# Kernel optimization log

Hardware: AMD Instinct MI355X
Metric: run time of the kernel (lower is better)

## Reference

```python
import jax, jax.numpy as jnp
import numpy as np

DIM = 1024
HEADS = 16
HEAD_DIM = DIM // HEADS
MLP = 4 * DIM
EPS = 1e-5


def layer_norm(x, g, b):
    mu = jnp.mean(x, axis=-1, keepdims=True)
    var = jnp.var(x, axis=-1, keepdims=True)
    return (x - mu) * jax.lax.rsqrt(var + EPS) * g + b


def rope_cos_sin(n, d):
    inv_freq = 1.0 / (10000.0 ** (jnp.arange(0, d, 2, dtype=jnp.float32) / d))
    t = jnp.arange(n, dtype=jnp.float32)
    freqs = jnp.outer(t, inv_freq)          # [N, d/2]
    emb = jnp.concatenate([freqs, freqs], -1)  # [N, d]
    return jnp.cos(emb), jnp.sin(emb)


def rotate_half(x):
    x1, x2 = x[..., ::2], x[..., 1::2]
    return jnp.concatenate([-x2, x1], axis=-1)


def setup_inputs() -> dict:
    key = jax.random.key(0)
    ks = jax.random.split(key, 16)
    B, N = 2, 2048
    s = lambda fan_in: 1.0 / np.sqrt(fan_in)
    inp = {
        "x": jax.random.normal(ks[0], (B, N, DIM), jnp.float32),
        "t_emb": jax.random.normal(ks[1], (B, DIM), jnp.float32),
        "norm1_g": jnp.ones((DIM,), jnp.float32),
        "norm1_b": jnp.zeros((DIM,), jnp.float32),
        "Wq": jax.random.normal(ks[2], (DIM, DIM), jnp.float32) * s(DIM),
        "Wk": jax.random.normal(ks[3], (DIM, DIM), jnp.float32) * s(DIM),
        "Wv": jax.random.normal(ks[4], (DIM, DIM), jnp.float32) * s(DIM),
        "Wo": jax.random.normal(ks[5], (DIM, DIM), jnp.float32) * s(DIM),
        "norm2_g": jnp.ones((DIM,), jnp.float32),
        "norm2_b": jnp.zeros((DIM,), jnp.float32),
        "W1": jax.random.normal(ks[6], (DIM, MLP), jnp.float32) * s(DIM),
        "W2": jax.random.normal(ks[7], (MLP, DIM), jnp.float32) * s(MLP),
        "ada_W": jax.random.normal(ks[8], (DIM, 6 * DIM), jnp.float32) * s(DIM),
        "ada_b": jnp.zeros((6 * DIM,), jnp.float32),
    }
    return inp


def reference(x, t_emb, norm1_g, norm1_b, Wq, Wk, Wv, Wo,
              norm2_g, norm2_b, W1, W2, ada_W, ada_b):
    B, N, C = x.shape
    H, D = HEADS, HEAD_DIM
    scale = D ** -0.5

    mod = jax.nn.silu(t_emb) @ ada_W + ada_b          # [B, 6C]
    (shift_msa, scale_msa, gate_msa,
     shift_mlp, scale_mlp, gate_mlp) = jnp.split(mod, 6, axis=-1)

    xn = layer_norm(x, norm1_g, norm1_b) * (1 + scale_msa[:, None, :]) + shift_msa[:, None, :]

    q = (xn @ Wq).reshape(B, N, H, D).transpose(0, 2, 1, 3)  # [B,H,N,D]
    k = (xn @ Wk).reshape(B, N, H, D).transpose(0, 2, 1, 3)
    v = (xn @ Wv).reshape(B, N, H, D).transpose(0, 2, 1, 3)

    cos, sin = rope_cos_sin(N, D)                     # [N, D]
    q = q * cos + rotate_half(q) * sin
    k = k * cos + rotate_half(k) * sin

    attn = jnp.einsum('bhnd,bhmd->bhnm', q, k) * scale  # explicit O(N^2) scores
    attn = jax.nn.softmax(attn, axis=-1)
    out = jnp.einsum('bhnm,bhmd->bhnd', attn, v)

    out = out.transpose(0, 2, 1, 3).reshape(B, N, C) @ Wo
    x = x + gate_msa[:, None, :] * out

    xn = layer_norm(x, norm2_g, norm2_b) * (1 + scale_mlp[:, None, :]) + shift_mlp[:, None, :]
    mlp = jax.nn.gelu(xn @ W1, approximate=False) @ W2
    x = x + gate_mlp[:, None, :] * mlp
    return x
```

## Files before the change

kernel.cpp:

```cpp
#include <hip/hip_runtime.h>
#include <math.h>

#define BB    2
#define NN    2048
#define CDIM  1024
#define HEADS 16
#define HDIM  64
#define MLPD  4096
#define MODC  6144
#define EPSV  1e-5f
#define LOG2E 1.4426950408889634f
#define MSPLIT 16

typedef __attribute__((ext_vector_type(8))) short s8v;
typedef __attribute__((ext_vector_type(4))) float f4v;

__device__ inline unsigned short f2bf(float f) {
  union { float f; unsigned u; } v; v.f = f;
  unsigned r = v.u + 0x7FFFu + ((v.u >> 16) & 1u);
  return (unsigned short)(r >> 16);
}
__device__ inline float bf2f(unsigned short h) {
  union { unsigned u; float f; } v; v.u = ((unsigned)h) << 16;
  return v.f;
}

__global__ __launch_bounds__(256) void mod_part(
    const float* __restrict__ t_emb, const float* __restrict__ ada_W,
    float* __restrict__ part) {
  int j = blockIdx.x * 256 + threadIdx.x;
  int b = blockIdx.y, ks = blockIdx.z;
  __shared__ float st[64];
  if (threadIdx.x < 64) {
    float v = t_emb[b * CDIM + ks * 64 + threadIdx.x];
    st[threadIdx.x] = v / (1.0f + expf(-v));
  }
  __syncthreads();
  float acc = 0.f;
  const float* wp = ada_W + (size_t)(ks * 64) * MODC + j;
  #pragma unroll 8
  for (int i = 0; i < 64; ++i) acc += st[i] * wp[(size_t)i * MODC];
  part[((size_t)ks * BB + b) * MODC + j] = acc;
}

__global__ __launch_bounds__(256) void mod_reduce(
    const float* __restrict__ part, const float* __restrict__ ada_b,
    float* __restrict__ mod) {
  int idx = blockIdx.x * 256 + threadIdx.x;
  int b = idx / MODC, j = idx % MODC;
  float a = ada_b[j];
  #pragma unroll
  for (int s = 0; s < MSPLIT; ++s) a += part[((size_t)s * BB + b) * MODC + j];
  mod[(size_t)b * MODC + j] = a;
}

__device__ inline float wave_sum64(float v) {
  for (int o = 32; o > 0; o >>= 1) v += __shfl_down(v, o, 64);
  return v;
}

__global__ __launch_bounds__(256) void ln_mod_bf16(
    const float* __restrict__ x, const float* __restrict__ g,
    const float* __restrict__ bta, const float* __restrict__ mod,
    int shift_off, int scale_off, unsigned short* __restrict__ out) {
  int r = blockIdx.x;
  int b = r / NN;
  int t = threadIdx.x;
  const float* xr = x + (size_t)r * CDIM;
  float4 xv = ((const float4*)xr)[t];
  float s  = xv.x + xv.y + xv.z + xv.w;
  float s2 = xv.x*xv.x + xv.y*xv.y + xv.z*xv.z + xv.w*xv.w;
  __shared__ float ws1[4], ws2[4];
  float sw = wave_sum64(s), s2w = wave_sum64(s2);
  int lane = t & 63, wid = t >> 6;
  if (lane == 0) { ws1[wid] = sw; ws2[wid] = s2w; }
  __syncthreads();
  float mu  = (ws1[0] + ws1[1] + ws1[2] + ws1[3]) * (1.0f / CDIM);
  float var = (ws2[0] + ws2[1] + ws2[2] + ws2[3]) * (1.0f / CDIM) - mu * mu;
  float rstd = rsqrtf(var + EPSV);
  const float* mods = mod + (size_t)b * MODC;
  float4 gv = ((const float4*)g)[t];
  float4 bv = ((const float4*)bta)[t];
  float4 sc = ((const float4*)(mods + scale_off))[t];
  float4 sh = ((const float4*)(mods + shift_off))[t];
  ushort4 ov;
  ov.x = f2bf(((xv.x - mu) * rstd * gv.x + bv.x) * (1.0f + sc.x) + sh.x);
  ov.y = f2bf(((xv.y - mu) * rstd * gv.y + bv.y) * (1.0f + sc.y) + sh.y);
  ov.z = f2bf(((xv.z - mu) * rstd * gv.z + bv.z) * (1.0f + sc.z) + sh.z);
  ov.w = f2bf(((xv.w - mu) * rstd * gv.w + bv.w) * (1.0f + sc.w) + sh.w);
  ((ushort4*)(out + (size_t)r * CDIM))[t] = ov;
}

__global__ __launch_bounds__(256) void wcast_all(
    const float* __restrict__ Wq, const float* __restrict__ Wk,
    const float* __restrict__ Wv, const float* __restrict__ Wo,
    const float* __restrict__ W1, const float* __restrict__ W2,
    unsigned short* __restrict__ Wqkvt, unsigned short* __restrict__ Wot,
    unsigned short* __restrict__ W1t, unsigned short* __restrict__ W2t) {
  int bid = blockIdx.x;
  const float* W; unsigned short* Wt; int K, N, t;
  if (bid < 4096) {
    int m = bid >> 10;
    t = bid & 1023;
    K = CDIM; N = CDIM;
    W  = (m == 0) ? Wq : (m == 1) ? Wk : (m == 2) ? Wv : Wo;
    Wt = (m == 3) ? Wot : (Wqkvt + (size_t)m * CDIM * CDIM);
  } else if (bid < 8192) {
    t = bid - 4096; K = CDIM; N = MLPD; W = W1; Wt = W1t;
  } else {
    t = bid - 8192; K = MLPD; N = CDIM; W = W2; Wt = W2t;
  }
  int ntiles = N >> 5;
  int n0 = (t % ntiles) * 32, k0 = (t / ntiles) * 32;
  __shared__ float tile[32][33];
  int tx = threadIdx.x & 31, ty = threadIdx.x >> 5;
  #pragma unroll
  for (int p = 0; p < 4; ++p)
    tile[ty + p * 8][tx] = W[(size_t)(k0 + ty + p * 8) * N + n0 + tx];
  __syncthreads();
  #pragma unroll
  for (int p = 0; p < 4; ++p)
    Wt[(size_t)(n0 + ty + p * 8) * K + k0 + tx] = f2bf(tile[tx][ty + p * 8]);
}

__global__ __launch_bounds__(1024) void mfma_gemm_big(
    const unsigned short* __restrict__ A,
    const unsigned short* __restrict__ Bt,
    int M, int N, int K,
    unsigned short* __restrict__ Ob, unsigned short* __restrict__ Ob2,
    unsigned short* __restrict__ Ob3, int mode) {
  __shared__ unsigned short SH[3 * 16384];
  int tid = threadIdx.x;
  int wave = tid >> 6, lane = tid & 63;
  int quad = lane >> 4, l15 = lane & 15;
  int m0 = blockIdx.y * 128, n0 = blockIdx.x * 128;
  int pos = wave & 7;
  int om = pos >> 1, on = pos & 1;
  int ks = wave >> 3;

  f4v acc[2][4] = {};

  int srow = lane >> 3;
  int ksrc = ((lane & 7) ^ (lane >> 3)) << 3;
  const int nt = K >> 6;

  #define STAGE_BIG(T, BUF)                                                    \
    {                                                                          \
      int k0_ = (T) << 6;                                                      \
      unsigned short* dsta = SH + (BUF) * 16384 + wave * 512;                  \
      const unsigned short* ga =                                               \
          A + (size_t)(m0 + 8 * wave + srow) * K + k0_ + ksrc;                 \
      __builtin_amdgcn_global_load_lds(                                        \
          (const __attribute__((address_space(1))) unsigned int*)(const void*)ga, \
          (__attribute__((address_space(3))) unsigned int*)(void*)dsta,        \
          16, 0, 0);                                                           \
      const unsigned short* gb =                                               \
          Bt + (size_t)(n0 + 8 * wave + srow) * K + k0_ + ksrc;                \
      __builtin_amdgcn_global_load_lds(                                        \
          (const __attribute__((address_space(1))) unsigned int*)(const void*)gb, \
          (__attribute__((address_space(3))) unsigned int*)(void*)(dsta + 8192), \
          16, 0, 0);                                                           \
    }

  STAGE_BIG(0, 0);
  STAGE_BIG(1, 1);
  asm volatile("s_waitcnt vmcnt(2)" ::: "memory");
  __syncthreads();

  int kx = (ks * 32 + quad * 8) ^ ((l15 & 7) << 3);

  int rbuf = 0, sbuf = 2;
  for (int t = 0; t < nt; ++t) {
    if (t + 2 < nt) STAGE_BIG(t + 2, sbuf);

    const unsigned short* base = SH + rbuf * 16384;
    s8v af[2], bf[4];
    #pragma unroll
    for (int i = 0; i < 2; ++i)
      af[i] = *(const s8v*)(base + (om * 32 + i * 16 + l15) * 64 + kx);
    #pragma unroll
    for (int j = 0; j < 4; ++j)
      bf[j] = *(const s8v*)(base + 8192 + (on * 64 + j * 16 + l15) * 64 + kx);
    #pragma unroll
    for (int i = 0; i < 2; ++i)
      #pragma unroll
      for (int j = 0; j < 4; ++j)
        acc[i][j] = __builtin_amdgcn_mfma_f32_16x16x32_bf16(
            af[i], bf[j], acc[i][j], 0, 0, 0);

    if (t + 2 < nt) {
      asm volatile("s_waitcnt vmcnt(2)" ::: "memory");
    } else if (t + 1 < nt) {
      asm volatile("s_waitcnt vmcnt(0)" ::: "memory");
    }
    __syncthreads();
    rbuf = (rbuf == 2) ? 0 : rbuf + 1;
    sbuf = (sbuf == 2) ? 0 : sbuf + 1;
  }
  #undef STAGE_BIG

  float* red = (float*)SH;
  if (wave >= 8) {
    int rb = (wave - 8) * 2304 + lane * 36;
    #pragma unroll
    for (int i = 0; i < 2; ++i)
      #pragma unroll
      for (int j = 0; j < 4; ++j)
        *(f4v*)(red + rb + (i * 4 + j) * 4) = acc[i][j];
  }
  __syncthreads();
  if (wave < 8) {
    int rb = wave * 2304 + lane * 36;
    #pragma unroll
    for (int i = 0; i < 2; ++i)
      #pragma unroll
      for (int j = 0; j < 4; ++j)
        acc[i][j] += *(const f4v*)(red + rb + (i * 4 + j) * 4);
    #pragma unroll
    for (int i = 0; i < 2; ++i) {
      int rbase = m0 + om * 32 + i * 16 + quad * 4;
      #pragma unroll
      for (int j = 0; j < 4; ++j) {
        int c = n0 + on * 64 + j * 16 + l15;
        #pragma unroll
        for (int rg = 0; rg < 4; ++rg) {
          int r = rbase + rg;
          float v = acc[i][j][rg];
          if (mode == 0) {
            unsigned short* dst = (c < 1024) ? Ob : ((c < 2048) ? Ob2 : Ob3);
            dst[(size_t)r * 1024 + (c & 1023)] = f2bf(v);
          } else {
            v = 0.5f * v * (1.0f + erff(v * 0.70710678118f));
            Ob[(size_t)r * N + c] = f2bf(v);
          }
        }
      }
    }
  }
}

__global__ __launch_bounds__(1024) void mfma_gemm_res(
    const unsigned short* __restrict__ A,
    const unsigned short* __restrict__ Bt,
    int M, int N, int K,
    float* __restrict__ O0,
    const float* __restrict__ res, const float* __restrict__ mod,
    int gate_off) {
  __shared__ unsigned short SH[3 * 16384];
  int tid = threadIdx.x;
  int wave = tid >> 6, lane = tid & 63;
  int quad = lane >> 4, l15 = lane & 15;
  int m0 = blockIdx.y * 128, n0 = blockIdx.x * 128;
  int pos = wave & 7;
  int om = pos >> 1, on = pos & 1;
  int ks = wave >> 3;

  f4v acc[2][4] = {};

  int srow = lane >> 3;
  int ksrc = ((lane & 7) ^ (lane >> 3)) << 3;
  const int nt = K >> 6;

  #define STAGE_RES(T, BUF)                                                    \
    {                                                                          \
      int k0_ = (T) << 6;                                                      \
      unsigned short* dsta = SH + (BUF) * 16384 + wave * 512;                  \
      const unsigned short* ga =                                               \
          A + (size_t)(m0 + 8 * wave + srow) * K + k0_ + ksrc;                 \
      __builtin_amdgcn_global_load_lds(                                        \
          (const __attribute__((address_space(1))) unsigned int*)(const void*)ga, \
          (__attribute__((address_space(3))) unsigned int*)(void*)dsta,        \
          16, 0, 0);                                                           \
      const unsigned short* gb =                                               \
          Bt + (size_t)(n0 + 8 * wave + srow) * K + k0_ + ksrc;                \
      __builtin_amdgcn_global_load_lds(                                        \
          (const __attribute__((address_space(1))) unsigned int*)(const void*)gb, \
          (__attribute__((address_space(3))) unsigned int*)(void*)(dsta + 8192), \
          16, 0, 0);                                                           \
    }

  STAGE_RES(0, 0);
  STAGE_RES(1, 1);
  asm volatile("s_waitcnt vmcnt(2)" ::: "memory");
  __syncthreads();

  int kx = (ks * 32 + quad * 8) ^ ((l15 & 7) << 3);

  int rbuf = 0, sbuf = 2;
  for (int t = 0; t < nt; ++t) {
    if (t + 2 < nt) STAGE_RES(t + 2, sbuf);

    const unsigned short* base = SH + rbuf * 16384;
    s8v af[2], bf[4];
    #pragma unroll
    for (int i = 0; i < 2; ++i)
      af[i] = *(const s8v*)(base + (om * 32 + i * 16 + l15) * 64 + kx);
    #pragma unroll
    for (int j = 0; j < 4; ++j)
      bf[j] = *(const s8v*)(base + 8192 + (on * 64 + j * 16 + l15) * 64 + kx);
    #pragma unroll
    for (int i = 0; i < 2; ++i)
      #pragma unroll
      for (int j = 0; j < 4; ++j)
        acc[i][j] = __builtin_amdgcn_mfma_f32_16x16x32_bf16(
            af[i], bf[j], acc[i][j], 0, 0, 0);

    if (t + 2 < nt) {
      asm volatile("s_waitcnt vmcnt(2)" ::: "memory");
    } else if (t + 1 < nt) {
      asm volatile("s_waitcnt vmcnt(0)" ::: "memory");
    }
    __syncthreads();
    rbuf = (rbuf == 2) ? 0 : rbuf + 1;
    sbuf = (sbuf == 2) ? 0 : sbuf + 1;
  }
  #undef STAGE_RES

  float* red = (float*)SH;
  if (wave >= 8) {
    int rb = (wave - 8) * 2304 + lane * 36;
    #pragma unroll
    for (int i = 0; i < 2; ++i)
      #pragma unroll
      for (int j = 0; j < 4; ++j)
        *(f4v*)(red + rb + (i * 4 + j) * 4) = acc[i][j];
  }
  __syncthreads();
  if (wave < 8) {
    int rb = wave * 2304 + lane * 36;
    #pragma unroll
    for (int i = 0; i < 2; ++i)
      #pragma unroll
      for (int j = 0; j < 4; ++j)
        acc[i][j] += *(const f4v*)(red + rb + (i * 4 + j) * 4);
    #pragma unroll
    for (int i = 0; i < 2; ++i) {
      int rbase = m0 + om * 32 + i * 16 + quad * 4;
      #pragma unroll
      for (int j = 0; j < 4; ++j) {
        int c = n0 + on * 64 + j * 16 + l15;
        #pragma unroll
        for (int rg = 0; rg < 4; ++rg) {
          int r = rbase + rg;
          int bb2 = r >> 11;
          O0[(size_t)r * N + c] =
              res[(size_t)r * N + c] + mod[bb2 * MODC + gate_off + c] * acc[i][j][rg];
        }
      }
    }
  }
}

__global__ __launch_bounds__(256) void rope_qk(
    unsigned short* __restrict__ qb, const unsigned short* __restrict__ kb,
    unsigned short* __restrict__ kpack, float qscale) {
  int r = blockIdx.x;
  int b = r / NN, n = r % NN;
  int t = threadIdx.x;
  int isK = blockIdx.y;
  const unsigned short* src = isK ? kb : qb;
  float scale = isK ? 1.0f : qscale;
  __shared__ float row[CDIM];
  __shared__ float csv[32], snv[32];
  if (t < 32) {
    float invf = powf(10000.0f, -(float)t / 32.0f);
    float sn, cs;
    sincosf((float)n * invf, &sn, &cs);
    csv[t] = cs * scale; snv[t] = sn * scale;
  }
  const unsigned short* qr = src + (size_t)r * CDIM;
  ushort4 xv = ((const ushort4*)qr)[t];
  row[t * 4 + 0] = bf2f(xv.x);
  row[t * 4 + 1] = bf2f(xv.y);
  row[t * 4 + 2] = bf2f(xv.z);
  row[t * 4 + 3] = bf2f(xv.w);
  __syncthreads();
  unsigned short o[4];
  int c0 = t * 4;
  #pragma unroll
  for (int q4 = 0; q4 < 4; ++q4) {
    int c = c0 + q4;
    int h = c >> 6, d = c & 63;
    int i = d & 31;
    float rh = (d < 32) ? -row[h * 64 + 2 * d + 1] : row[h * 64 + 2 * (d - 32)];
    o[q4] = f2bf(row[c] * csv[i] + rh * snv[i]);
  }
  if (!isK) {
    ((ushort4*)(qb + (size_t)r * CDIM))[t] = make_ushort4(o[0], o[1], o[2], o[3]);
  } else {
    int h = c0 >> 6, d0 = c0 & 63;
    int half = d0 >> 5, quad = (d0 >> 3) & 3, j0 = d0 & 7;
    int bh = b * HEADS + h;
    int tt = n >> 6, kt = (n >> 4) & 3, l15 = n & 15;
    int lane = quad * 16 + l15;
    size_t off = ((((size_t)bh * 32 + tt) * 8 + kt * 2 + half) * 64 + lane) * 8 + j0;
    unsigned int lo = (unsigned)o[0] | ((unsigned)o[1] << 16);
    unsigned int hi = (unsigned)o[2] | ((unsigned)o[3] << 16);
    *(uint2*)(kpack + off) = make_uint2(lo, hi);
  }
}

__global__ __launch_bounds__(256) void vtrans_pack(
    const unsigned short* __restrict__ vrow, unsigned short* __restrict__ vpack) {
  int t = blockIdx.x;
  int bh = blockIdx.y;
  int b = bh >> 4, h = bh & 15;
  __shared__ unsigned short L[64 * 72];
  int tid = threadIdx.x;
  #pragma unroll
  for (int p = 0; p < 2; ++p) {
    int c = tid + p * 256;
    int key = c >> 3, dc = (c & 7) * 8;
    *(s8v*)(L + key * 72 + dc) =
        *(const s8v*)(vrow + (size_t)(b * NN + t * 64 + key) * CDIM + h * HDIM + dc);
  }
  __syncthreads();
  #pragma unroll
  for (int p = 0; p < 2; ++p) {
    int o = tid + p * 256;
    int f = o >> 6, lane = o & 63;
    int dt = f >> 1, half = f & 1, quad = lane >> 4, l15 = lane & 15;
    int d = dt * 16 + l15;
    unsigned short tmp[8];
    #pragma unroll
    for (int j = 0; j < 8; ++j) {
      int key = (j & 3) * 16 + half * 8 + quad * 2 + (j >> 2);
      tmp[j] = L[key * 72 + d];
    }
    *(s8v*)(vpack + ((((size_t)bh * 32 + t) * 8 + f) * 64 + lane) * 8) = *(s8v*)tmp;
  }
}

__global__ __launch_bounds__(512, 4) void fattn_pack(
    const unsigned short* __restrict__ qb,
    const unsigned short* __restrict__ kpack,
    const unsigned short* __restrict__ vpack,
    unsigned short* __restrict__ ob) {
  int bid = blockIdx.x;
  int qt = bid >> 5, bh = bid & 31;
  int b = bh >> 4, h = bh & 15;
  int tid = threadIdx.x;
  int wave = tid >> 6, lane = tid & 63;
  int quad = lane >> 4, l15 = lane & 15;

  __shared__ unsigned short smem[16384 + 8 * 1152];
  unsigned short* Pw = smem + 16384 + wave * 1152;

  int n0 = qt * 128;
  int qrow = n0 + wave * 16 + l15;
  s8v qf[2];
  {
    const unsigned short* qp = qb + (size_t)(b * NN + qrow) * CDIM + h * HDIM;
    qf[0] = *(const s8v*)(qp + quad * 8);
    qf[1] = *(const s8v*)(qp + 32 + quad * 8);
  }

  f4v acc[4] = {};
  float m_i[4], l_i[4];
  #pragma unroll
  for (int r = 0; r < 4; ++r) { m_i[r] = -1e30f; l_i[r] = 0.f; }

  const unsigned short* ksrc = kpack + (size_t)bh * 131072 + wave * 512 + lane * 8;
  const unsigned short* vsrc = vpack + (size_t)bh * 131072 + wave * 512 + lane * 8;

  #define STAGE_ATT(T, BUF)                                                    \
    {                                                                          \
      __builtin_amdgcn_global_load_lds(                                        \
          (const __attribute__((address_space(1))) unsigned int*)(const void*)(ksrc + (size_t)(T) * 4096), \
          (__attribute__((address_space(3))) unsigned int*)(void*)(smem + (BUF) * 8192 + wave * 512), \
          16, 0, 0);                                                           \
      __builtin_amdgcn_global_load_lds(                                        \
          (const __attribute__((address_space(1))) unsigned int*)(const void*)(vsrc + (size_t)(T) * 4096), \
          (__attribute__((address_space(3))) unsigned int*)(void*)(smem + (BUF) * 8192 + 4096 + wave * 512), \
          16, 0, 0);                                                           \
    }

  STAGE_ATT(0, 0);
  asm volatile("s_waitcnt vmcnt(0)" ::: "memory");
  __syncthreads();

  int buf = 0;
  for (int t = 0; t < NN / 64; ++t) {
    if (t + 1 < NN / 64) STAGE_ATT(t + 1, buf ^ 1);

    const unsigned short* kb_ = smem + buf * 8192 + lane * 8;
    const unsigned short* vb_ = kb_ + 4096;
    s8v kf[8], vf[8];
    #pragma unroll
    for (int f = 0; f < 8; ++f) kf[f] = *(const s8v*)(kb_ + f * 512);
    #pragma unroll
    for (int f = 0; f < 8; ++f) vf[f] = *(const s8v*)(vb_ + f * 512);

    f4v s4[4] = {};
    #pragma unroll
    for (int kt = 0; kt < 4; ++kt) {
      s4[kt] = __builtin_amdgcn_mfma_f32_16x16x32_bf16(qf[0], kf[kt * 2], s4[kt], 0, 0, 0);
      s4[kt] = __builtin_amdgcn_mfma_f32_16x16x32_bf16(qf[1], kf[kt * 2 + 1], s4[kt], 0, 0, 0);
    }

    #pragma unroll
    for (int r = 0; r < 4; ++r) {
      float mv = fmaxf(fmaxf(s4[0][r], s4[1][r]), fmaxf(s4[2][r], s4[3][r]));
      #pragma unroll
      for (int msk = 1; msk < 16; msk <<= 1)
        mv = fmaxf(mv, __shfl_xor(mv, msk, 64));
      float mnew = fmaxf(m_i[r], mv);
      float alpha = __builtin_amdgcn_exp2f(m_i[r] - mnew);
      m_i[r] = mnew;
      float ls = 0.f;
      #pragma unroll
      for (int kt = 0; kt < 4; ++kt) {
        float p = __builtin_amdgcn_exp2f(s4[kt][r] - mnew);
        s4[kt][r] = p;
        ls += p;
      }
      l_i[r] = l_i[r] * alpha + ls;
      acc[0][r] *= alpha; acc[1][r] *= alpha;
      acc[2][r] *= alpha; acc[3][r] *= alpha;
    }

    #pragma unroll
    for (int r = 0; r < 4; ++r) {
      unsigned int lo = (__float_as_uint(s4[0][r]) >> 16) |
                        (__float_as_uint(s4[1][r]) & 0xffff0000u);
      unsigned int hi = (__float_as_uint(s4[2][r]) >> 16) |
                        (__float_as_uint(s4[3][r]) & 0xffff0000u);
      *(uint2*)(Pw + (quad * 4 + r) * 72 + l15 * 4) = make_uint2(lo, hi);
    }

    s8v pf0 = *(const s8v*)(Pw + l15 * 72 + quad * 8);
    s8v pf1 = *(const s8v*)(Pw + l15 * 72 + 32 + quad * 8);

    #pragma unroll
    for (int dt = 0; dt < 4; ++dt) {
      acc[dt] = __builtin_amdgcn_mfma_f32_16x16x32_bf16(pf0, vf[dt * 2], acc[dt], 0, 0, 0);
      acc[dt] = __builtin_amdgcn_mfma_f32_16x16x32_bf16(pf1, vf[dt * 2 + 1], acc[dt], 0, 0, 0);
    }

    if (t + 1 < NN / 64) {
      asm volatile("s_waitcnt vmcnt(0)" ::: "memory");
      __syncthreads();
      buf ^= 1;
    }
  }
  #undef STAGE_ATT

  #pragma unroll
  for (int r = 0; r < 4; ++r) {
    float l = l_i[r];
    #pragma unroll
    for (int msk = 1; msk < 16; msk <<= 1)
      l += __shfl_xor(l, msk, 64);
    float inv = 1.0f / l;
    size_t row = (size_t)(b * NN + n0 + wave * 16 + quad * 4 + r);
    unsigned short* op = ob + row * CDIM + h * HDIM;
    #pragma unroll
    for (int dt = 0; dt < 4; ++dt)
      op[dt * 16 + l15] = f2bf(acc[dt][r] * inv);
  }
}

extern "C" void kernel_launch(void* const* d_in, const int* in_sizes, int n_in,
                              void* d_out, int out_size, void* d_ws, size_t ws_size,
                              hipStream_t stream) {
  const float* x    = (const float*)d_in[0];
  const float* temb = (const float*)d_in[1];
  const float* n1g  = (const float*)d_in[2];
  const float* n1b  = (const float*)d_in[3];
  const float* Wq   = (const float*)d_in[4];
  const float* Wk   = (const float*)d_in[5];
  const float* Wv   = (const float*)d_in[6];
  const float* Wo   = (const float*)d_in[7];
  const float* n2g  = (const float*)d_in[8];
  const float* n2b  = (const float*)d_in[9];
  const float* W1   = (const float*)d_in[10];
  const float* W2   = (const float*)d_in[11];
  const float* adaW = (const float*)d_in[12];
  const float* adab = (const float*)d_in[13];
  float* out = (float*)d_out;

  const size_t TOK = (size_t)BB * NN * CDIM;
  float* wsf = (float*)d_ws;
  float* mod     = wsf;
  float* modpart = wsf + 16384;
  unsigned short* tokb  = (unsigned short*)(wsf + 16384 + MSPLIT * BB * MODC);
  unsigned short* qb    = tokb + TOK;
  unsigned short* kb    = qb + TOK;
  unsigned short* kpack = kb + TOK;
  unsigned short* vpack = kpack + TOK;
  unsigned short* Wqkvt = vpack + TOK;
  unsigned short* Wot   = Wqkvt + 3 * CDIM * CDIM;
  unsigned short* W1t   = Wot + CDIM * CDIM;
  unsigned short* W2t   = W1t + CDIM * MLPD;
  unsigned short* h1b   = W2t + MLPD * CDIM;
  unsigned short* vrow  = h1b;
  float* x1 = (float*)qb;

  const int M = BB * NN;

  mod_part<<<dim3(MODC / 256, BB, MSPLIT), 256, 0, stream>>>(temb, adaW, modpart);
  mod_reduce<<<dim3(BB * MODC / 256), 256, 0, stream>>>(modpart, adab, mod);
  ln_mod_bf16<<<dim3(M), 256, 0, stream>>>(x, n1g, n1b, mod, 0, 1024, tokb);

  wcast_all<<<dim3(12288), 256, 0, stream>>>(
      Wq, Wk, Wv, Wo, W1, W2, Wqkvt, Wot, W1t, W2t);

  mfma_gemm_big<<<dim3(24, 32), 1024, 0, stream>>>(
      tokb, Wqkvt, M, 3 * CDIM, CDIM, qb, kb, vrow, 0);

  rope_qk<<<dim3(M, 2), 256, 0, stream>>>(qb, kb, kpack, 0.125f * LOG2E);

  vtrans_pack<<<dim3(NN / 64, BB * HEADS), 256, 0, stream>>>(vrow, vpack);

  fattn_pack<<<dim3((NN / 128) * BB * HEADS), 512, 0, stream>>>(
      qb, kpack, vpack, tokb);

  mfma_gemm_res<<<dim3(CDIM / 128, M / 128), 1024, 0, stream>>>(
      tokb, Wot, M, CDIM, CDIM, x1, x, mod, 2048);

  ln_mod_bf16<<<dim3(M), 256, 0, stream>>>(x1, n2g, n2b, mod, 3072, 4096, tokb);

  mfma_gemm_big<<<dim3(MLPD / 128, M / 128), 1024, 0, stream>>>(
      tokb, W1t, M, MLPD, CDIM, h1b, nullptr, nullptr, 1);

  mfma_gemm_res<<<dim3(CDIM / 128, M / 128), 1024, 0, stream>>>(
      h1b, W2t, M, CDIM, MLPD, out, x1, mod, 5120);
}
```

Measured before the change: 428.7 us.

## Process two 16-row query fragments per wave in flash attention

Each wave now handles 32 query rows instead of 16, so a block covers 256 queries and reuses every staged K/V tile for twice as many rows. This halves the number of blocks and the total global-to-LDS K/V traffic. In exchange it raises register use per thread (launch bounds occupancy hint dropped) and per-block LDS for the P buffers. The grid shrinks to 256 blocks, which is close to the CU count and may leave less latency hiding.

Result: no change. 428.8 us (+0.0%).

```diff
diff --git a/kernel.cpp b/kernel.cpp
--- a/kernel.cpp
+++ b/kernel.cpp
@@ -431,7 +431,7 @@
   }
 }
 
-__global__ __launch_bounds__(512, 4) void fattn_pack(
+__global__ __launch_bounds__(512) void fattn_pack(
     const unsigned short* __restrict__ qb,
     const unsigned short* __restrict__ kpack,
     const unsigned short* __restrict__ vpack,
@@ -443,22 +443,25 @@
   int wave = tid >> 6, lane = tid & 63;
   int quad = lane >> 4, l15 = lane & 15;
 
-  __shared__ unsigned short smem[16384 + 8 * 1152];
-  unsigned short* Pw = smem + 16384 + wave * 1152;
-
-  int n0 = qt * 128;
-  int qrow = n0 + wave * 16 + l15;
-  s8v qf[2];
-  {
+  __shared__ unsigned short smem[16384 + 8 * 2304];
+  unsigned short* Pw = smem + 16384 + wave * 2304;
+
+  int n0 = qt * 256;
+  s8v qf[2][2];
+  #pragma unroll
+  for (int fq = 0; fq < 2; ++fq) {
+    int qrow = n0 + wave * 32 + fq * 16 + l15;
     const unsigned short* qp = qb + (size_t)(b * NN + qrow) * CDIM + h * HDIM;
-    qf[0] = *(const s8v*)(qp + quad * 8);
-    qf[1] = *(const s8v*)(qp + 32 + quad * 8);
-  }
-
-  f4v acc[4] = {};
-  float m_i[4], l_i[4];
-  #pragma unroll
-  for (int r = 0; r < 4; ++r) { m_i[r] = -1e30f; l_i[r] = 0.f; }
+    qf[fq][0] = *(const s8v*)(qp + quad * 8);
+    qf[fq][1] = *(const s8v*)(qp + 32 + quad * 8);
+  }
+
+  f4v acc[2][4] = {};
+  float m_i[2][4], l_i[2][4];
+  #pragma unroll
+  for (int fq = 0; fq < 2; ++fq)
+    #pragma unroll
+    for (int r = 0; r < 4; ++r) { m_i[fq][r] = -1e30f; l_i[fq][r] = 0.f; }
 
   const unsigned short* ksrc = kpack + (size_t)bh * 131072 + wave * 512 + lane * 8;
   const unsigned short* vsrc = vpack + (size_t)bh * 131072 + wave * 512 + lane * 8;
@@ -484,57 +487,72 @@
     if (t + 1 < NN / 64) STAGE_ATT(t + 1, buf ^ 1);
 
     const unsigned short* kb_ = smem + buf * 8192 + lane * 8;
-    const unsigned short* vb_ = kb_ + 4096;
-    s8v kf[8], vf[8];
-    #pragma unroll
-    for (int f = 0; f < 8; ++f) kf[f] = *(const s8v*)(kb_ + f * 512);
-    #pragma unroll
-    for (int f = 0; f < 8; ++f) vf[f] = *(const s8v*)(vb_ + f * 512);
-
-    f4v s4[4] = {};
-    #pragma unroll
-    for (int kt = 0; kt < 4; ++kt) {
-      s4[kt] = __builtin_amdgcn_mfma_f32_16x16x32_bf16(qf[0], kf[kt * 2], s4[kt], 0, 0, 0);
-      s4[kt] = __builtin_amdgcn_mfma_f32_16x16x32_bf16(qf[1], kf[kt * 2 + 1], s4[kt], 0, 0, 0);
-    }
-
-    #pragma unroll
-    for (int r = 0; r < 4; ++r) {
-      float mv = fmaxf(fmaxf(s4[0][r], s4[1][r]), fmaxf(s4[2][r], s4[3][r]));
-      #pragma unroll
-      for (int msk = 1; msk < 16; msk <<= 1)
-        mv = fmaxf(mv, __shfl_xor(mv, msk, 64));
-      float mnew = fmaxf(m_i[r], mv);
-      float alpha = __builtin_amdgcn_exp2f(m_i[r] - mnew);
-      m_i[r] = mnew;
-      float ls = 0.f;
-      #pragma unroll
-      for (int kt = 0; kt < 4; ++kt) {
-        float p = __builtin_amdgcn_exp2f(s4[kt][r] - mnew);
-        s4[kt][r] = p;
-        ls += p;
+    f4v s4[2][4];
+    {
+      s8v kf[8];
+      #pragma unroll
+      for (int f = 0; f < 8; ++f) kf[f] = *(const s8v*)(kb_ + f * 512);
+      #pragma unroll
+      for (int fq = 0; fq < 2; ++fq)
+        #pragma unroll
+        for (int kt = 0; kt < 4; ++kt) {
+          f4v z = {};
+          z = __builtin_amdgcn_mfma_f32_16x16x32_bf16(qf[fq][0], kf[kt * 2], z, 0, 0, 0);
+          z = __builtin_amdgcn_mfma_f32_16x16x32_bf16(qf[fq][1], kf[kt * 2 + 1], z, 0, 0, 0);
+          s4[fq][kt] = z;
+        }
+    }
+
+    #pragma unroll
+    for (int fq = 0; fq < 2; ++fq)
+      #pragma unroll
+      for (int r = 0; r < 4; ++r) {
+        float mv = fmaxf(fmaxf(s4[fq][0][r], s4[fq][1][r]),
+                         fmaxf(s4[fq][2][r], s4[fq][3][r]));
+        #pragma unroll
+        for (int msk = 1; msk < 16; msk <<= 1)
+          mv = fmaxf(mv, __shfl_xor(mv, msk, 64));
+        float mnew = fmaxf(m_i[fq][r], mv);
+        float alpha = __builtin_amdgcn_exp2f(m_i[fq][r] - mnew);
+        m_i[fq][r] = mnew;
+        float ls = 0.f;
+        #pragma unroll
+        for (int kt = 0; kt < 4; ++kt) {
+          float p = __builtin_amdgcn_exp2f(s4[fq][kt][r] - mnew);
+          s4[fq][kt][r] = p;
+          ls += p;
+        }
+        l_i[fq][r] = l_i[fq][r] * alpha + ls;
+        acc[fq][0][r] *= alpha; acc[fq][1][r] *= alpha;
+        acc[fq][2][r] *= alpha; acc[fq][3][r] *= alpha;
       }
-      l_i[r] = l_i[r] * alpha + ls;
-      acc[0][r] *= alpha; acc[1][r] *= alpha;
-      acc[2][r] *= alpha; acc[3][r] *= alpha;
-    }
-
-    #pragma unroll
-    for (int r = 0; r < 4; ++r) {
-      unsigned int lo = (__float_as_uint(s4[0][r]) >> 16) |
-                        (__float_as_uint(s4[1][r]) & 0xffff0000u);
-      unsigned int hi = (__float_as_uint(s4[2][r]) >> 16) |
-                        (__float_as_uint(s4[3][r]) & 0xffff0000u);
-      *(uint2*)(Pw + (quad * 4 + r) * 72 + l15 * 4) = make_uint2(lo, hi);
-    }
-
-    s8v pf0 = *(const s8v*)(Pw + l15 * 72 + quad * 8);
-    s8v pf1 = *(const s8v*)(Pw + l15 * 72 + 32 + quad * 8);
-
-    #pragma unroll
-    for (int dt = 0; dt < 4; ++dt) {
-      acc[dt] = __builtin_amdgcn_mfma_f32_16x16x32_bf16(pf0, vf[dt * 2], acc[dt], 0, 0, 0);
-      acc[dt] = __builtin_amdgcn_mfma_f32_16x16x32_bf16(pf1, vf[dt * 2 + 1], acc[dt], 0, 0, 0);
+
+    #pragma unroll
+    for (int fq = 0; fq < 2; ++fq)
+      #pragma unroll
+      for (int r = 0; r < 4; ++r) {
+        unsigned int lo = (__float_as_uint(s4[fq][0][r]) >> 16) |
+                          (__float_as_uint(s4[fq][1][r]) & 0xffff0000u);
+        unsigned int hi = (__float_as_uint(s4[fq][2][r]) >> 16) |
+                          (__float_as_uint(s4[fq][3][r]) & 0xffff0000u);
+        *(uint2*)(Pw + (fq * 16 + quad * 4 + r) * 72 + l15 * 4) = make_uint2(lo, hi);
+      }
+
+    {
+      const unsigned short* vb_ = smem + buf * 8192 + 4096 + lane * 8;
+      s8v vf[8];
+      #pragma unroll
+      for (int f = 0; f < 8; ++f) vf[f] = *(const s8v*)(vb_ + f * 512);
+      #pragma unroll
+      for (int fq = 0; fq < 2; ++fq) {
+        s8v pf0 = *(const s8v*)(Pw + (fq * 16 + l15) * 72 + quad * 8);
+        s8v pf1 = *(const s8v*)(Pw + (fq * 16 + l15) * 72 + 32 + quad * 8);
+        #pragma unroll
+        for (int dt = 0; dt < 4; ++dt) {
+          acc[fq][dt] = __builtin_amdgcn_mfma_f32_16x16x32_bf16(pf0, vf[dt * 2], acc[fq][dt], 0, 0, 0);
+          acc[fq][dt] = __builtin_amdgcn_mfma_f32_16x16x32_bf16(pf1, vf[dt * 2 + 1], acc[fq][dt], 0, 0, 0);
+        }
+      }
     }
 
     if (t + 1 < NN / 64) {
@@ -546,18 +564,20 @@
   #undef STAGE_ATT
 
   #pragma unroll
-  for (int r = 0; r < 4; ++r) {
-    float l = l_i[r];
-    #pragma unroll
-    for (int msk = 1; msk < 16; msk <<= 1)
-      l += __shfl_xor(l, msk, 64);
-    float inv = 1.0f / l;
-    size_t row = (size_t)(b * NN + n0 + wave * 16 + quad * 4 + r);
-    unsigned short* op = ob + row * CDIM + h * HDIM;
-    #pragma unroll
-    for (int dt = 0; dt < 4; ++dt)
-      op[dt * 16 + l15] = f2bf(acc[dt][r] * inv);
-  }
+  for (int fq = 0; fq < 2; ++fq)
+    #pragma unroll
+    for (int r = 0; r < 4; ++r) {
+      float l = l_i[fq][r];
+      #pragma unroll
+      for (int msk = 1; msk < 16; msk <<= 1)
+        l += __shfl_xor(l, msk, 64);
+      float inv = 1.0f / l;
+      size_t row = (size_t)(b * NN + n0 + wave * 32 + fq * 16 + quad * 4 + r);
+      unsigned short* op = ob + row * CDIM + h * HDIM;
+      #pragma unroll
+      for (int dt = 0; dt < 4; ++dt)
+        op[dt * 16 + l15] = f2bf(acc[fq][dt][r] * inv);
+    }
 }
 
 extern "C" void kernel_launch(void* const* d_in, const int* in_sizes, int n_in,
@@ -612,7 +632,7 @@
 
   vtrans_pack<<<dim3(NN / 64, BB * HEADS), 256, 0, stream>>>(vrow, vpack);
 
-  fattn_pack<<<dim3((NN / 128) * BB * HEADS), 512, 0, stream>>>(
+  fattn_pack<<<dim3((NN / 256) * BB * HEADS), 512, 0, stream>>>(
       qb, kpack, vpack, tokb);
 
   mfma_gemm_res<<<dim3(CDIM / 128, M / 128), 1024, 0, stream>>>(
```
